# Optimization experiments

Measured on AMD Instinct MI355X. Metric: run time of the kernel, lower is better.

## Reference

```python
import jax, jax.numpy as jnp
import numpy as np

MODES1 = 12
MODES2 = 12
IN_CH = 32
OUT_CH = 32
B, H, W = 16, 256, 256
SCALE = 1.0 / (IN_CH * OUT_CH)


def setup_inputs() -> dict:
    key = jax.random.key(0)
    k1, k2, k3 = jax.random.split(key, 3)
    x = jax.random.normal(k1, (B, IN_CH, H, W), dtype=jnp.float32)
    w1 = SCALE * jax.random.uniform(k2, (IN_CH, OUT_CH, MODES1, MODES2, 2), dtype=jnp.float32)
    w2 = SCALE * jax.random.uniform(k3, (IN_CH, OUT_CH, MODES1, MODES2, 2), dtype=jnp.float32)
    return {"x": x, "weights1": w1, "weights2": w2}


def _compl_mul2d(inp, w):
    # inp: [b,i,x,y] complex ; w: [i,o,x,y,2] real -> complex
    wc = jax.lax.complex(w[..., 0], w[..., 1])
    return jnp.einsum('bixy,ioxy->boxy', inp, wc)


def reference(x, weights1, weights2):
    H_, W_ = x.shape[-2], x.shape[-1]
    m1 = min(MODES1, H_ // 2)
    m2 = min(MODES2, W_ // 2 + 1)
    x_ft = jnp.fft.rfft2(x.astype(jnp.float32))  # [B, Cin, H, W//2+1]
    low = _compl_mul2d(x_ft[:, :, :m1, :m2], weights1[:, :, :m1, :m2])
    high = _compl_mul2d(x_ft[:, :, -m1:, :m2], weights2[:, :, :m1, :m2])
    out_ft = jnp.zeros((x.shape[0], OUT_CH, H_, W_ // 2 + 1), dtype=jnp.complex64)
    out_ft = out_ft.at[:, :, :m1, :m2].set(low)
    out_ft = out_ft.at[:, :, H_ - m1:, :m2].set(high)
    return jnp.fft.irfft2(out_ft, s=(H_, W_)).astype(x.dtype)
```

## Files before the change

### kernel.cpp

```cpp
#include <hip/hip_runtime.h>


#define TPI 6.28318530717958647692f

__global__ __launch_bounds__(256, 2) void k12_hwdft(const float* __restrict__ x,
                                                    float* __restrict__ Xf) {
  __shared__ float2 step2[64];
  __shared__ float red[4 * 13 * 128];
  __shared__ float2 Ys2[13 * 130];
  const int blk = blockIdx.x;
  const int bi = blk >> 1, wh = blk & 1;
  const int t = threadIdx.x;
  const int q = t >> 6, l = t & 63;

  if (t < 64) {
    float s, c;
    sincosf(TPI * (float)t * (1.0f / 256.0f), &s, &c);
    step2[t] = make_float2(c, s);
  }
  __syncthreads();

  const float2* xp2 = reinterpret_cast<const float2*>(x + (size_t)bi * 65536 + wh * 128) + l;
  float2 aC[13], aS12[12];
#pragma unroll
  for (int j = 0; j < 13; j++) aC[j] = make_float2(0.f, 0.f);
#pragma unroll
  for (int j = 0; j < 12; j++) aS12[j] = make_float2(0.f, 0.f);

  const int h0 = q * 16;
  float2 c0 = xp2[h0 * 128];
  float2 c1 = xp2[(h0 + 64) * 128];
  float2 c2 = xp2[(h0 + 128) * 128];
  float2 c3 = xp2[(h0 + 192) * 128];
#pragma unroll 4
  for (int hh = 0; hh < 16; hh++) {
    int h = h0 + hh;
    int hn = h0 + ((hh + 1) & 15);
    float2 n0 = xp2[hn * 128];
    float2 n1 = xp2[(hn + 64) * 128];
    float2 n2 = xp2[(hn + 128) * 128];
    float2 n3 = xp2[(hn + 192) * 128];
    float2 p02 = make_float2(c0.x + c2.x, c0.y + c2.y);
    float2 m02 = make_float2(c0.x - c2.x, c0.y - c2.y);
    float2 p13 = make_float2(c1.x + c3.x, c1.y + c3.y);
    float2 m13 = make_float2(c1.x - c3.x, c1.y - c3.y);
    float2 A = make_float2(p02.x + p13.x, p02.y + p13.y);
    float2 Bv = make_float2(p02.x - p13.x, p02.y - p13.y);
    aC[0].x += A.x; aC[0].y += A.y;
    float2 st = step2[h];
    float cj = st.x, sj = st.y;
#pragma unroll
    for (int jj = 0; jj < 12; jj++) {
      const int j = jj + 1, r = j & 3;
      if (r == 0) {
        aC[j].x = fmaf(A.x, cj, aC[j].x);   aC[j].y = fmaf(A.y, cj, aC[j].y);
        aS12[jj].x = fmaf(A.x, sj, aS12[jj].x); aS12[jj].y = fmaf(A.y, sj, aS12[jj].y);
      } else if (r == 2) {
        aC[j].x = fmaf(Bv.x, cj, aC[j].x);  aC[j].y = fmaf(Bv.y, cj, aC[j].y);
        aS12[jj].x = fmaf(Bv.x, sj, aS12[jj].x); aS12[jj].y = fmaf(Bv.y, sj, aS12[jj].y);
      } else if (r == 1) {
        aC[j].x = fmaf(m02.x, cj, fmaf(-m13.x, sj, aC[j].x));
        aC[j].y = fmaf(m02.y, cj, fmaf(-m13.y, sj, aC[j].y));
        aS12[jj].x = fmaf(m02.x, sj, fmaf(m13.x, cj, aS12[jj].x));
        aS12[jj].y = fmaf(m02.y, sj, fmaf(m13.y, cj, aS12[jj].y));
      } else {
        aC[j].x = fmaf(m02.x, cj, fmaf(m13.x, sj, aC[j].x));
        aC[j].y = fmaf(m02.y, cj, fmaf(m13.y, sj, aC[j].y));
        aS12[jj].x = fmaf(m02.x, sj, fmaf(-m13.x, cj, aS12[jj].x));
        aS12[jj].y = fmaf(m02.y, sj, fmaf(-m13.y, cj, aS12[jj].y));
      }
      if (jj < 11) {
        float nc = fmaf(cj, st.x, -(sj * st.y));
        float ns = fmaf(cj, st.y, sj * st.x);
        cj = nc; sj = ns;
      }
    }
    c0 = n0; c1 = n1; c2 = n2; c3 = n3;
  }

  for (int p = 0; p < 2; p++) {
    __syncthreads();
#pragma unroll
    for (int cc = 0; cc < 13; cc++) {
      int cls = p * 13 + cc;
      int j = cls >> 1;
      float2 v;
      if (cls & 1) v = (j == 0) ? make_float2(0.f, 0.f) : aS12[j - 1];
      else v = aC[j];
      *reinterpret_cast<float2*>(&red[(q * 13 + cc) * 128 + 2 * l]) = v;
    }
    __syncthreads();
    for (int idx = t; idx < 13 * 128; idx += 256) {
      int cc = idx >> 7, wl = idx & 127;
      int cls = p * 13 + cc;
      float s = red[(0 * 13 + cc) * 128 + wl] + red[(1 * 13 + cc) * 128 + wl] +
                red[(2 * 13 + cc) * 128 + wl] + red[(3 * 13 + cc) * 128 + wl];
      if (cls & 1) Ys2[(cls >> 1) * 130 + wl].y = s;
      else         Ys2[(cls >> 1) * 130 + wl].x = s;
    }
  }
  __syncthreads();

  if (t < 156) {
    int j = t / 12, kx = t % 12;
    float c1p, s1p, c2p, s2p;
    {
      float s, c;
      sincosf(TPI * (float)kx * (1.0f / 256.0f), &s, &c);
      c1p = c; s1p = -s;
      sincosf(TPI * (float)((2 * kx) & 255) * (1.0f / 256.0f), &s, &c);
      c2p = c; s2p = -s;
    }
    const float2* CS = &Ys2[j * 130];
    float pr0 = 1.0f, pi0 = 0.0f;
    float pr1 = c1p, pi1 = s1p;
    float A = 0, B = 0, D = 0, E = 0;
#pragma unroll 4
    for (int w = 0; w < 128; w += 2) {
      float4 vv = *reinterpret_cast<const float4*>(&CS[w]);
      A = fmaf(vv.x, pr0, A); B = fmaf(vv.x, pi0, B);
      D = fmaf(vv.y, pr0, D); E = fmaf(vv.y, pi0, E);
      A = fmaf(vv.z, pr1, A); B = fmaf(vv.z, pi1, B);
      D = fmaf(vv.w, pr1, D); E = fmaf(vv.w, pi1, E);
      float n0r = pr0 * c2p - pi0 * s2p, n0i = pr0 * s2p + pi0 * c2p;
      float n1r = pr1 * c2p - pi1 * s2p, n1i = pr1 * s2p + pi1 * c2p;
      pr0 = n0r; pi0 = n0i; pr1 = n1r; pi1 = n1i;
    }
    float sgn = (wh && (kx & 1)) ? -1.0f : 1.0f;
    A *= sgn; B *= sgn; D *= sgn; E *= sgn;
    float2* Xo = reinterpret_cast<float2*>(Xf) + (size_t)wh * 147456;
    size_t base = (size_t)kx * 512 + bi;
    if (j <= 11) Xo[(size_t)j * 6144 + base] = make_float2(A + E, B - D);
    if (j >= 1)  Xo[(size_t)(24 - j) * 6144 + base] = make_float2(A - E, B + D);
  }
}

__global__ __launch_bounds__(256) void k3_mix(const float* __restrict__ Xf,
                                              const float* __restrict__ w1,
                                              const float* __restrict__ w2,
                                              float* __restrict__ Ff) {
  __shared__ float Xs[1024];
  __shared__ float Ws[2048];
  int m = blockIdx.x;
  int ky = m / 12, kx = m % 12;
  int t = threadIdx.x;
  const float* Xsl = Xf + (size_t)m * 1024;
  for (int e = t; e < 1024; e += 256) Xs[e] = Xsl[e] + Xsl[e + 294912];
  const float* Wp = (ky < 12) ? w1 : w2;
  int myr = (ky < 12) ? ky : ky - 12;
  int woff = myr * 24 + kx * 2;
  for (int e = t; e < 1024; e += 256) {
    float2 wv = *reinterpret_cast<const float2*>(Wp + (size_t)e * 288 + woff);
    Ws[e * 2] = wv.x; Ws[e * 2 + 1] = wv.y;
  }
  __syncthreads();
  int o = t & 31, bh = t >> 5;
  float ar = 0, ai = 0, br = 0, bi_ = 0;
#pragma unroll
  for (int i = 0; i < 32; i++) {
    float wr = Ws[i * 64 + o * 2], wi = Ws[i * 64 + o * 2 + 1];
    float x1r = Xs[bh * 64 + i * 2], x1i = Xs[bh * 64 + i * 2 + 1];
    float x2r = Xs[(bh + 8) * 64 + i * 2], x2i = Xs[(bh + 8) * 64 + i * 2 + 1];
    ar = fmaf(x1r, wr, ar); ar = fmaf(-x1i, wi, ar);
    ai = fmaf(x1r, wi, ai); ai = fmaf(x1i, wr, ai);
    br = fmaf(x2r, wr, br); br = fmaf(-x2i, wi, br);
    bi_ = fmaf(x2r, wi, bi_); bi_ = fmaf(x2i, wr, bi_);
  }
  float scale = (kx == 0 ? 1.0f : 2.0f) * (1.0f / 65536.0f);
  float2* Fo = reinterpret_cast<float2*>(Ff) + (size_t)m * 512;
  Fo[(size_t)bh * 32 + o] = make_float2(ar * scale, ai * scale);
  Fo[(size_t)(bh + 8) * 32 + o] = make_float2(br * scale, bi_ * scale);
}

__global__ __launch_bounds__(256) void k45_inv(const float* __restrict__ Ff,
                                               float* __restrict__ out) {
  __shared__ float tw[128 * 27];
  __shared__ float PQ[13 * 12 * 4];
  __shared__ float Gs[256 * 24];
  const int bo = blockIdx.x;
  const int t = threadIdx.x;
  const int l = t & 63, wq = t >> 6;

  for (int e = t; e < 128 * 13; e += 256) {
    int h = e / 13, j = e % 13;
    float s, c;
    sincosf(TPI * (float)((h * j) & 255) * (1.0f / 256.0f), &s, &c);
    tw[h * 27 + 2 * j] = c;
    tw[h * 27 + 2 * j + 1] = s;
  }
  if (t < 156) {
    int j = t / 12, kx = t % 12;
    const float2* F2 = reinterpret_cast<const float2*>(Ff);
    float lr = 0, li = 0, hr = 0, hi = 0;
    if (j < 12) { float2 v = F2[((size_t)j * 12 + kx) * 512 + bo]; lr = v.x; li = v.y; }
    if (j > 0)  { float2 v = F2[((size_t)(24 - j) * 12 + kx) * 512 + bo]; hr = v.x; hi = v.y; }
    PQ[(j * 12 + kx) * 4 + 0] = lr + hr;
    PQ[(j * 12 + kx) * 4 + 1] = li + hi;
    PQ[(j * 12 + kx) * 4 + 2] = hi - li;
    PQ[(j * 12 + kx) * 4 + 3] = lr - hr;
  }
  __syncthreads();

  if (t < 192) {
    const int kx = t % 12, hq = t / 12;
    float Pr[13], Pi[13], Qr[13], Qi[13];
#pragma unroll
    for (int j = 0; j < 13; j++) {
      Pr[j] = PQ[(j * 12 + kx) * 4 + 0];
      Pi[j] = PQ[(j * 12 + kx) * 4 + 1];
      Qr[j] = PQ[(j * 12 + kx) * 4 + 2];
      Qi[j] = PQ[(j * 12 + kx) * 4 + 3];
    }
    for (int hh = 0; hh < 8; hh++) {
      int h = hh * 16 + hq;
      float Er = 0, Ei = 0, Or = 0, Oi = 0;
#pragma unroll
      for (int j = 0; j < 13; j++) {
        float c = tw[h * 27 + 2 * j], s = tw[h * 27 + 2 * j + 1];
        if (j & 1) {
          Or = fmaf(Pr[j], c, Or); Or = fmaf(Qr[j], s, Or);
          Oi = fmaf(Pi[j], c, Oi); Oi = fmaf(Qi[j], s, Oi);
        } else {
          Er = fmaf(Pr[j], c, Er); Er = fmaf(Qr[j], s, Er);
          Ei = fmaf(Pi[j], c, Ei); Ei = fmaf(Qi[j], s, Ei);
        }
      }
      Gs[h * 24 + 2 * kx] = Er + Or;
      Gs[h * 24 + 2 * kx + 1] = Ei + Oi;
      Gs[(h + 128) * 24 + 2 * kx] = Er - Or;
      Gs[(h + 128) * 24 + 2 * kx + 1] = Ei - Oi;
    }
  }

  float cA[12], sA[12], cB[12], sB[12];
#pragma unroll
  for (int kx = 1; kx < 12; kx++) {
    float s, c;
    __sincosf(TPI * (float)((kx * (2 * l)) & 255) * (1.0f / 256.0f), &s, &c);
    cA[kx] = c; sA[kx] = s;
    __sincosf(TPI * (float)((kx * (2 * l + 1)) & 255) * (1.0f / 256.0f), &s, &c);
    cB[kx] = c; sB[kx] = s;
  }
  __syncthreads();

  float* ob0 = out + ((size_t)bo * 256 + wq * 64) * 256;
  for (int rs = 0; rs < 64; rs++) {
    int rl = wq * 64 + rs;
    float g[24];
    const float4* gr4 = reinterpret_cast<const float4*>(&Gs[rl * 24]);
#pragma unroll
    for (int qq = 0; qq < 6; qq++) {
      float4 v = gr4[qq];
      g[4 * qq] = v.x; g[4 * qq + 1] = v.y; g[4 * qq + 2] = v.z; g[4 * qq + 3] = v.w;
    }
    float E0 = g[0], O0 = 0, E1 = g[0], O1 = 0;
#pragma unroll
    for (int kx = 1; kx < 12; kx++) {
      float ta = g[2 * kx] * cA[kx] - g[2 * kx + 1] * sA[kx];
      float tb = g[2 * kx] * cB[kx] - g[2 * kx + 1] * sB[kx];
      if (kx & 1) { O0 += ta; O1 += tb; } else { E0 += ta; E1 += tb; }
    }
    float* orow = ob0 + rs * 256;
    float2 v0 = make_float2(E0 + O0, E1 + O1);
    float2 v1 = make_float2(E0 - O0, E1 - O1);
    __builtin_nontemporal_store(*reinterpret_cast<double*>(&v0),
                                reinterpret_cast<double*>(&orow[2 * l]));
    __builtin_nontemporal_store(*reinterpret_cast<double*>(&v1),
                                reinterpret_cast<double*>(&orow[128 + 2 * l]));
  }
}

extern "C" void kernel_launch(void* const* d_in, const int* in_sizes, int n_in,
                              void* d_out, int out_size, void* d_ws, size_t ws_size,
                              hipStream_t stream) {
  const float* x = (const float*)d_in[0];
  const float* w1 = (const float*)d_in[1];
  const float* w2 = (const float*)d_in[2];
  float* out = (float*)d_out;
  float* ws = (float*)d_ws;

  float* Xf = ws;
  float* Ff = ws + 589824;

  k12_hwdft<<<1024, 256, 0, stream>>>(x, Xf);
  k3_mix<<<288, 256, 0, stream>>>(Xf, w1, w2, Ff);
  k45_inv<<<512, 256, 0, stream>>>(Ff, out);
}
```

Before: 73.12 us.

## Fuse spectral channel mixing into inverse DFT kernel and drop separate mix launch

Removes the standalone mixing kernel and has each inverse-transform block compute its own 288 mixed modes for its (batch, out-channel) pair directly from the forward spectrum and weights. This removes a kernel launch and the intermediate buffer write/read. In exchange, each block redundantly reads spectrum and strided weight data from global memory without shared-memory reuse, serialising a 32-step loop per thread before the inverse transform starts.

```diff
diff --git a/kernel.cpp b/kernel.cpp
--- a/kernel.cpp
+++ b/kernel.cpp
@@ -135,51 +135,18 @@
   }
 }
 
-__global__ __launch_bounds__(256) void k3_mix(const float* __restrict__ Xf,
-                                              const float* __restrict__ w1,
-                                              const float* __restrict__ w2,
-                                              float* __restrict__ Ff) {
-  __shared__ float Xs[1024];
-  __shared__ float Ws[2048];
-  int m = blockIdx.x;
-  int ky = m / 12, kx = m % 12;
-  int t = threadIdx.x;
-  const float* Xsl = Xf + (size_t)m * 1024;
-  for (int e = t; e < 1024; e += 256) Xs[e] = Xsl[e] + Xsl[e + 294912];
-  const float* Wp = (ky < 12) ? w1 : w2;
-  int myr = (ky < 12) ? ky : ky - 12;
-  int woff = myr * 24 + kx * 2;
-  for (int e = t; e < 1024; e += 256) {
-    float2 wv = *reinterpret_cast<const float2*>(Wp + (size_t)e * 288 + woff);
-    Ws[e * 2] = wv.x; Ws[e * 2 + 1] = wv.y;
-  }
-  __syncthreads();
-  int o = t & 31, bh = t >> 5;
-  float ar = 0, ai = 0, br = 0, bi_ = 0;
-#pragma unroll
-  for (int i = 0; i < 32; i++) {
-    float wr = Ws[i * 64 + o * 2], wi = Ws[i * 64 + o * 2 + 1];
-    float x1r = Xs[bh * 64 + i * 2], x1i = Xs[bh * 64 + i * 2 + 1];
-    float x2r = Xs[(bh + 8) * 64 + i * 2], x2i = Xs[(bh + 8) * 64 + i * 2 + 1];
-    ar = fmaf(x1r, wr, ar); ar = fmaf(-x1i, wi, ar);
-    ai = fmaf(x1r, wi, ai); ai = fmaf(x1i, wr, ai);
-    br = fmaf(x2r, wr, br); br = fmaf(-x2i, wi, br);
-    bi_ = fmaf(x2r, wi, bi_); bi_ = fmaf(x2i, wr, bi_);
-  }
-  float scale = (kx == 0 ? 1.0f : 2.0f) * (1.0f / 65536.0f);
-  float2* Fo = reinterpret_cast<float2*>(Ff) + (size_t)m * 512;
-  Fo[(size_t)bh * 32 + o] = make_float2(ar * scale, ai * scale);
-  Fo[(size_t)(bh + 8) * 32 + o] = make_float2(br * scale, bi_ * scale);
-}
-
-__global__ __launch_bounds__(256) void k45_inv(const float* __restrict__ Ff,
+__global__ __launch_bounds__(256) void k45_inv(const float* __restrict__ Xf,
+                                               const float* __restrict__ w1,
+                                               const float* __restrict__ w2,
                                                float* __restrict__ out) {
   __shared__ float tw[128 * 27];
+  __shared__ float2 Fs[288];
   __shared__ float PQ[13 * 12 * 4];
   __shared__ float Gs[256 * 24];
   const int bo = blockIdx.x;
   const int t = threadIdx.x;
   const int l = t & 63, wq = t >> 6;
+  const int b = bo >> 5, o = bo & 31;
 
   for (int e = t; e < 128 * 13; e += 256) {
     int h = e / 13, j = e % 13;
@@ -188,12 +155,33 @@
     tw[h * 27 + 2 * j] = c;
     tw[h * 27 + 2 * j + 1] = s;
   }
+
+  for (int m = t; m < 288; m += 256) {
+    int ky = m / 12, kx = m % 12;
+    const float* Wp = (ky < 12) ? w1 : w2;
+    int myr = (ky < 12) ? ky : ky - 12;
+    int woff = myr * 24 + kx * 2;
+    const float2* Xm = reinterpret_cast<const float2*>(Xf) + (size_t)m * 512 + b * 32;
+    float ar = 0, ai = 0;
+#pragma unroll 8
+    for (int i = 0; i < 32; i++) {
+      float2 x0 = Xm[i];
+      float2 x1 = Xm[i + 147456];
+      float xr = x0.x + x1.x, xi = x0.y + x1.y;
+      float2 wv = *reinterpret_cast<const float2*>(Wp + ((size_t)i * 32 + o) * 288 + woff);
+      ar = fmaf(xr, wv.x, fmaf(-xi, wv.y, ar));
+      ai = fmaf(xr, wv.y, fmaf(xi, wv.x, ai));
+    }
+    float scale = (kx == 0 ? 1.0f : 2.0f) * (1.0f / 65536.0f);
+    Fs[m] = make_float2(ar * scale, ai * scale);
+  }
+  __syncthreads();
+
   if (t < 156) {
     int j = t / 12, kx = t % 12;
-    const float2* F2 = reinterpret_cast<const float2*>(Ff);
     float lr = 0, li = 0, hr = 0, hi = 0;
-    if (j < 12) { float2 v = F2[((size_t)j * 12 + kx) * 512 + bo]; lr = v.x; li = v.y; }
-    if (j > 0)  { float2 v = F2[((size_t)(24 - j) * 12 + kx) * 512 + bo]; hr = v.x; hi = v.y; }
+    if (j < 12) { float2 v = Fs[j * 12 + kx]; lr = v.x; li = v.y; }
+    if (j > 0)  { float2 v = Fs[(24 - j) * 12 + kx]; hr = v.x; hi = v.y; }
     PQ[(j * 12 + kx) * 4 + 0] = lr + hr;
     PQ[(j * 12 + kx) * 4 + 1] = li + hi;
     PQ[(j * 12 + kx) * 4 + 2] = hi - li;
@@ -280,9 +268,7 @@
   float* ws = (float*)d_ws;
 
   float* Xf = ws;
-  float* Ff = ws + 589824;
 
   k12_hwdft<<<1024, 256, 0, stream>>>(x, Xf);
-  k3_mix<<<288, 256, 0, stream>>>(Xf, w1, w2, Ff);
-  k45_inv<<<512, 256, 0, stream>>>(Ff, out);
+  k45_inv<<<512, 256, 0, stream>>>(Xf, w1, w2, out);
 }
```

Measured after the change: 77.17 us. 5.5% more time.
